# Kernel tuning notes

Measured on AMD Instinct MI355X. Metric: run time of the kernel, lower is better.

Reference implementation:

```python
import jax, jax.numpy as jnp
import numpy as np
from jax import lax


def _dct_basis():
    # 64 separable 2D DCT-II basis filters, shape [64,1,8,8] (OIHW)
    k = 8
    a = np.full(k, np.sqrt(2.0 / k)); a[0] = np.sqrt(1.0 / k)
    u = np.arange(k)[:, None]; xx = np.arange(k)[None, :]
    B = a[:, None] * np.cos((2 * xx + 1) * u * np.pi / (2 * k))  # [u, x]
    basis = np.einsum('ux,vy->uvxy', B, B).reshape(64, 1, k, k)
    return jnp.asarray(basis, dtype=jnp.float32)


def _conv(x, w, b, pad):
    y = lax.conv_general_dilated(x, w, (1, 1), [(pad, pad), (pad, pad)],
                                 dimension_numbers=('NCHW', 'OIHW', 'NCHW'))
    return y + b[None, :, None, None]


def _bn(x, s, b, m, v, eps=1e-5):
    inv = s * lax.rsqrt(v + eps)
    return x * inv[None, :, None, None] + (b - m * inv)[None, :, None, None]


def _mp2(x):
    return lax.reduce_window(x, -jnp.inf, lax.max, (1, 1, 2, 2), (1, 1, 2, 2), 'VALID')


def setup_inputs() -> dict:
    key = jax.random.key(0)
    ks = jax.random.split(key, 32)
    B = 128
    d = {}
    d['x'] = jax.random.normal(ks[0], (B, 1, 256, 256), jnp.float32)
    d['qvectors'] = jax.random.uniform(ks[1], (B, 64), jnp.float32)
    d['dct_basis'] = _dct_basis()
    def w(k, shape, sc=0.02):
        return jax.random.normal(k, shape, jnp.float32) * sc
    # conv stack
    d['conv1a_w'] = w(ks[2], (64, 1, 5, 5));   d['conv1a_b'] = w(ks[3], (64,))
    d['conv1b_w'] = w(ks[4], (64, 64, 5, 5));  d['conv1b_b'] = w(ks[5], (64,))
    d['conv2a_w'] = w(ks[6], (128, 64, 5, 5)); d['conv2a_b'] = w(ks[7], (128,))
    d['conv3a_w'] = w(ks[8], (256, 128, 5, 5)); d['conv3a_b'] = w(ks[9], (256,))
    # batchnorm (eval-mode) params: scale, bias, running_mean, running_var
    for i, (name, c) in enumerate([('bn1a', 64), ('bn1b', 64), ('bn2a', 128), ('bn3a', 256)]):
        kk = jax.random.split(ks[10 + i], 4)
        d[name + '_s'] = 1.0 + w(kk[0], (c,))
        d[name + '_b'] = w(kk[1], (c,))
        d[name + '_m'] = w(kk[2], (c,))
        d[name + '_v'] = jax.random.uniform(kk[3], (c,), jnp.float32, 0.5, 1.5)
    d['fc1_w'] = w(ks[20], (500, 15 * 8 * 256 + 64), 0.01); d['fc1_b'] = w(ks[21], (500,))
    d['fc2_w'] = w(ks[22], (500, 564), 0.01);               d['fc2_b'] = w(ks[23], (500,))
    d['fc3_w'] = w(ks[24], (2, 564), 0.01);                 d['fc3_b'] = w(ks[25], (2,))
    return d


def reference(x, qvectors, dct_basis,
              conv1a_w, conv1a_b, bn1a_s, bn1a_b, bn1a_m, bn1a_v,
              conv1b_w, conv1b_b, bn1b_s, bn1b_b, bn1b_m, bn1b_v,
              conv2a_w, conv2a_b, bn2a_s, bn2a_b, bn2a_m, bn2a_v,
              conv3a_w, conv3a_b, bn3a_s, bn3a_b, bn3a_m, bn3a_v,
              fc1_w, fc1_b, fc2_w, fc2_b, fc3_w, fc3_b):
    gamma = 1e6
    # --- soft-histogram over DCT coefficients (no_grad in the original) ---
    dct = lax.conv_general_dilated(x, dct_basis, (8, 8), 'VALID',
                                   dimension_numbers=('NCHW', 'OIHW', 'NCHW'))  # [B,64,32,32]
    bins = jnp.arange(-60, 61, dtype=jnp.float32)  # 121 bins

    def step(_, b):
        s = jnp.sum(jax.nn.sigmoid(gamma * (dct - b)), axis=(2, 3)) / 1024.0  # [B,64]
        return None, s
    _, feats = lax.scan(step, None, bins)           # [121,B,64]
    feats = jnp.transpose(feats, (1, 0, 2))          # [B,121,64]
    features = feats[:, 0:120, :] - feats[:, 1:121, :]
    features = lax.stop_gradient(features.reshape(-1, 1, 120, 64))

    # --- CNN backbone ---
    h = jax.nn.relu(_bn(_conv(features, conv1a_w, conv1a_b, 2), bn1a_s, bn1a_b, bn1a_m, bn1a_v))
    h = jax.nn.relu(_bn(_conv(h, conv1b_w, conv1b_b, 2), bn1b_s, bn1b_b, bn1b_m, bn1b_v))
    h = _mp2(h)
    h = jax.nn.relu(_bn(_conv(h, conv2a_w, conv2a_b, 2), bn2a_s, bn2a_b, bn2a_m, bn2a_v))
    h = _mp2(h)
    h = jax.nn.relu(_bn(_conv(h, conv3a_w, conv3a_b, 2), bn3a_s, bn3a_b, bn3a_m, bn3a_v))
    h = _mp2(h)                                      # [B,256,15,8]
    h_flat = h.reshape(-1, 15 * 8 * 256)
    h = jnp.concatenate([qvectors, h_flat], axis=1)
    h = jax.nn.relu(h @ fc1_w.T + fc1_b)
    h = jnp.concatenate([qvectors, h], axis=1)
    h = jax.nn.relu(h @ fc2_w.T + fc2_b)
    h = jnp.concatenate([qvectors, h], axis=1)
    return h @ fc3_w.T + fc3_b
```

## Files before the change

kernel.cpp:

```cpp
#include <hip/hip_runtime.h>


typedef _Float16 half8 __attribute__((ext_vector_type(8)));
typedef _Float16 half4 __attribute__((ext_vector_type(4)));
typedef float f32x16 __attribute__((ext_vector_type(16)));

__device__ __forceinline__ void async_copy16(const void* g, void* l) {
  __builtin_amdgcn_global_load_lds(
      (__attribute__((address_space(1))) void*)g,
      (__attribute__((address_space(3))) void*)l, 16, 0, 0);
}

__global__ __launch_bounds__(256) void dct_kernel(const float* __restrict__ x,
                                                  const float* __restrict__ basis,
                                                  float* __restrict__ dct) {
  __shared__ __align__(16) float Bm[64];
  int tid = threadIdx.x;
  if (tid < 64) {
    int u = tid >> 3, xx = tid & 7;
    Bm[tid] = basis[(u * 8) * 64 + xx * 8] * 2.8284271247461903f;
  }
  __syncthreads();
  int gid = blockIdx.x * 256 + tid;
  int b = gid >> 10, blk = gid & 1023;
  int bi = blk >> 5, bj = blk & 31;
  const float* xp = x + (size_t)b * 65536 + (bi * 8) * 256 + bj * 8;
  float X[64];
#pragma unroll
  for (int r = 0; r < 8; ++r) {
    float4 p = *(const float4*)(xp + r * 256);
    float4 q = *(const float4*)(xp + r * 256 + 4);
    X[r * 8 + 0] = p.x; X[r * 8 + 1] = p.y; X[r * 8 + 2] = p.z; X[r * 8 + 3] = p.w;
    X[r * 8 + 4] = q.x; X[r * 8 + 5] = q.y; X[r * 8 + 6] = q.z; X[r * 8 + 7] = q.w;
  }
  float T[64];
#pragma unroll
  for (int u = 0; u < 8; ++u) {
    float t[8] = {0.f, 0.f, 0.f, 0.f, 0.f, 0.f, 0.f, 0.f};
#pragma unroll
    for (int xx = 0; xx < 8; ++xx) {
      float bm = Bm[u * 8 + xx];
#pragma unroll
      for (int y = 0; y < 8; ++y) t[y] += bm * X[xx * 8 + y];
    }
#pragma unroll
    for (int y = 0; y < 8; ++y) T[u * 8 + y] = t[y];
  }
  float* op = dct + (size_t)b * 65536 + bi * 32 + bj;
#pragma unroll
  for (int v = 0; v < 8; ++v) {
    float dc[8] = {0.f, 0.f, 0.f, 0.f, 0.f, 0.f, 0.f, 0.f};
#pragma unroll
    for (int y = 0; y < 8; ++y) {
      float bm = Bm[v * 8 + y];
#pragma unroll
      for (int u = 0; u < 8; ++u) dc[u] += bm * T[u * 8 + y];
    }
#pragma unroll
    for (int u = 0; u < 8; ++u) op[(u * 8 + v) * 1024] = dc[u];
  }
}

__global__ __launch_bounds__(256) void hist_kernel(const float* __restrict__ dct,
                                                   float* __restrict__ feat) {
  __shared__ __align__(16) float h[16 * 121];
  int tid = threadIdx.x;
  for (int i = tid; i < 16 * 121; i += 256) h[i] = 0.f;
  __syncthreads();
  int b = blockIdx.x >> 6, c = blockIdx.x & 63;
  const float* dp = dct + (size_t)(b * 64 + c) * 1024;
  float* hc = h + (tid & 15) * 121;
  float4 v4 = ((const float4*)dp)[tid];
  float vals[4] = {v4.x, v4.y, v4.z, v4.w};
#pragma unroll
  for (int i = 0; i < 4; ++i) {
    float d = vals[i];
    float fl = floorf(d);
    float t0 = d - fl;
    int k = (int)fl + 60;
    if (t0 >= 2e-5f && t0 <= 1.f - 1.2e-4f) {
      if (k >= 0 && k < 120) atomicAdd(hc + k, 1.0f);
    } else {
      float s0 = 1.f / (1.f + expf(-1e6f * t0));
      float s1 = 1.f / (1.f + expf(1e6f * (1.f - t0)));
      if (k >= 1 && k <= 120) atomicAdd(hc + k - 1, 1.f - s0);
      if (k >= 0 && k < 120)  atomicAdd(hc + k, s0 - s1);
      if (k >= -1 && k < 119) atomicAdd(hc + k + 1, s1);
    }
  }
  __syncthreads();
  for (int f = tid; f < 120; f += 256) {
    float s = 0.f;
#pragma unroll
    for (int l = 0; l < 16; ++l) s += h[l * 121 + f];
    feat[((size_t)b * 120 + f) * 64 + c] = s * (1.f / 1024.f);
  }
}

template <int CI, int CO>
__global__ __launch_bounds__(256) void wtrans(const float* __restrict__ w,
                                              _Float16* __restrict__ wt) {
  int i = blockIdx.x * 256 + threadIdx.x;
  if (i >= (CI / 8) * 26 * CO * 8) return;
  int c8 = i & 7;
  int t = i >> 3;
  int co = t % CO; t /= CO;
  int k = t % 26;
  int cg = t / 26;
  int ci = cg * 8 + c8;
  float v = (k < 25) ? w[((size_t)co * CI + ci) * 25 + k] : 0.f;
  wt[i] = (_Float16)v;
}

__global__ __launch_bounds__(256) void bnprep(const float* __restrict__ cb,
                                              const float* __restrict__ s,
                                              const float* __restrict__ b,
                                              const float* __restrict__ m,
                                              const float* __restrict__ v,
                                              float* __restrict__ scale,
                                              float* __restrict__ shift, int n) {
  int i = threadIdx.x;
  if (i < n) {
    float inv = s[i] * rsqrtf(v[i] + 1e-5f);
    scale[i] = inv;
    shift[i] = (cb[i] - m[i]) * inv + b[i];
  }
}

__global__ __launch_bounds__(256) void conv1a_f16(
    const float* __restrict__ in, const float* __restrict__ wts,
    const float* __restrict__ cb, const float* __restrict__ s_,
    const float* __restrict__ b_, const float* __restrict__ m_,
    const float* __restrict__ v_, _Float16* __restrict__ out) {
  __shared__ __align__(16) float wl[5 * 8 * 20];
  __shared__ __align__(16) float il[12 * 68];
  int tid = threadIdx.x, bid = blockIdx.x;
  int img = bid / 30;
  int r = bid % 30;
  int cob = r / 15;
  int h0 = (r % 15) * 8;
  int cog = tid & 7, wg = (tid >> 3) & 3, hh = tid >> 5;
  float acc[4][16];
#pragma unroll
  for (int i = 0; i < 4; ++i)
#pragma unroll
    for (int j = 0; j < 16; ++j) acc[i][j] = 0.f;
  for (int idx = tid; idx < 32 * 25; idx += 256) {
    int rr = idx % 25, co = idx / 25;
    float v = wts[(cob * 32 + co) * 25 + rr];
    int kh = rr / 5, kw = rr % 5;
    wl[(kh * 8 + (co >> 2)) * 20 + (co & 3) * 5 + kw] = v;
  }
  for (int idx = tid; idx < 12 * 68; idx += 256) {
    int cc = idx % 68, rr = idx / 68;
    int hy = h0 + rr - 2, wx = cc - 2;
    float v = 0.f;
    if (hy >= 0 && hy < 120 && wx >= 0 && wx < 64)
      v = in[(size_t)img * 7680 + hy * 64 + wx];
    il[idx] = v;
  }
  __syncthreads();
#pragma unroll
  for (int kh = 0; kh < 5; ++kh) {
    const float* ir = &il[(hh + kh) * 68 + wg * 16];
    float iv[20];
#pragma unroll
    for (int i = 0; i < 5; ++i) {
      float4 p = *(const float4*)(ir + i * 4);
      iv[i * 4] = p.x; iv[i * 4 + 1] = p.y; iv[i * 4 + 2] = p.z; iv[i * 4 + 3] = p.w;
    }
    const float* wr = &wl[(kh * 8 + cog) * 20];
    float wv[20];
#pragma unroll
    for (int i = 0; i < 5; ++i) {
      float4 p = *(const float4*)(wr + i * 4);
      wv[i * 4] = p.x; wv[i * 4 + 1] = p.y; wv[i * 4 + 2] = p.z; wv[i * 4 + 3] = p.w;
    }
#pragma unroll
    for (int co = 0; co < 4; ++co)
#pragma unroll
      for (int kw = 0; kw < 5; ++kw) {
        float w1 = wv[co * 5 + kw];
#pragma unroll
        for (int w = 0; w < 16; ++w) acc[co][w] += w1 * iv[w + kw];
      }
  }
  int h = h0 + hh;
  int co0 = cob * 32 + cog * 4;
  float inv[4], bia[4];
#pragma unroll
  for (int i = 0; i < 4; ++i) {
    int c = co0 + i;
    inv[i] = s_[c] * rsqrtf(v_[c] + 1e-5f);
    bia[i] = (cb[c] - m_[c]) * inv[i] + b_[c];
  }
  int g = co0 >> 3, off = co0 & 7;
  _Float16* op = out + (((size_t)(img * 8 + g) * 120 + h) * 64) * 8 + off;
#pragma unroll
  for (int w = 0; w < 16; ++w) {
    half4 o;
#pragma unroll
    for (int i = 0; i < 4; ++i)
      o[i] = (_Float16)fmaxf(acc[i][w] * inv[i] + bia[i], 0.f);
    *(half4*)&op[(size_t)(wg * 16 + w) * 8] = o;
  }
}

template <int CI, int CO, int H, int W, int BLK_M, bool OUT_NCHW, bool DBUF>
__global__ __launch_bounds__(512) void conv5_mfma(
    const _Float16* __restrict__ in, const _Float16* __restrict__ wt,
    const float* __restrict__ scale, const float* __restrict__ shift,
    _Float16* __restrict__ out) {
  constexpr int NW_M = BLK_M / 64;
  constexpr int NW_N = 8 / NW_M;
  constexpr int BLK_N = NW_N * 128;
  constexpr int ROWS = BLK_N / W;
  constexpr int TB = (H + ROWS - 1) / ROWS;
  constexpr int NCOB = CO / BLK_M;
  constexpr int HR = ROWS + 4;
  constexpr int HC = W + 4;
  constexpr int CIG = CI / 8;
  constexpr int OH = H / 2, OW = W / 2;
  constexpr int AITER = (HR * HC + 511) / 512;
  constexpr int WBYTES = 26 * BLK_M * 16;
  constexpr int WITER = (WBYTES + 8191) / 8192;
  constexpr int NBUF = DBUF ? 2 : 1;
  constexpr int ASZ = HR * HC * 8;
  constexpr int WSZ = 26 * BLK_M * 8;
  __shared__ __align__(16) _Float16 Alds[NBUF][ASZ];
  __shared__ __align__(16) _Float16 Wlds[NBUF][WSZ];

  int tid = threadIdx.x;
  int bid = blockIdx.x;
  int img = bid / (TB * NCOB);
  int r = bid % (TB * NCOB);
  int tb = r / NCOB;
  int cob = r % NCOB;
  int h0 = tb * ROWS;

  int wid = tid >> 6, l = tid & 63, lo = l & 31, hi = l >> 5;
  int widM = wid / NW_N, widN = wid % NW_N;

  int wbase[2];
#pragma unroll
  for (int mi = 0; mi < 2; ++mi)
    wbase[mi] = (hi * BLK_M + widM * 64 + mi * 32 + lo) * 8;
  int bbase[4];
#pragma unroll
  for (int j = 0; j < 4; ++j) {
    int pix = widN * 128 + j * 32 + lo;
    bbase[j] = ((pix / W) * HC + (pix % W)) * 8;
  }

  f32x16 acc[2][4];
#pragma unroll
  for (int mi = 0; mi < 2; ++mi)
#pragma unroll
    for (int j = 0; j < 4; ++j) acc[mi][j] = (f32x16){};

  auto loadA = [&](int cg, half8* areg) {
    const _Float16* ing = in + (size_t)(img * CIG + cg) * H * W * 8;
#pragma unroll
    for (int it = 0; it < AITER; ++it) {
      int i = tid + it * 512;
      half8 v = {};
      if (i < HR * HC) {
        int rr = i / HC, cc = i % HC;
        int hy = h0 + rr - 2, wx = cc - 2;
        if (hy >= 0 && hy < H && wx >= 0 && wx < W)
          v = *(const half8*)&ing[(size_t)(hy * W + wx) * 8];
      }
      areg[it] = v;
    }
  };
  auto issueW = [&](int cg, int buf) {
    const char* wsrc = (const char*)(wt + ((size_t)cg * 26 * CO + cob * BLK_M) * 8);
#pragma unroll
    for (int rr = 0; rr < WITER; ++rr) {
      int f = rr * 8192 + tid * 16;
      if (f < WBYTES) {
        int row = f / (BLK_M * 16);
        int off = f % (BLK_M * 16);
        async_copy16(wsrc + (size_t)row * (CO * 16) + off,
                     (char*)&Wlds[buf][0] + (rr * 8192 + wid * 1024));
      }
    }
  };
  auto writeA = [&](int buf, half8* areg) {
#pragma unroll
    for (int it = 0; it < AITER; ++it) {
      int i = tid + it * 512;
      if (i < HR * HC) *(half8*)&Alds[buf][i * 8] = areg[it];
    }
  };
  auto ldfrag = [&](int buf, int p, half8 (&af)[2], half8 (&bf)[4]) {
    int pos0 = 2 * p, pos1 = 2 * p + 1;
    int off0 = (pos0 / 5) * HC + (pos0 % 5);
    int off1 = (pos1 < 25) ? (pos1 / 5) * HC + (pos1 % 5) : 0;
    int off = (hi ? off1 : off0) * 8;
#pragma unroll
    for (int mi = 0; mi < 2; ++mi)
      af[mi] = *(const half8*)&Wlds[buf][wbase[mi] + pos0 * BLK_M * 8];
#pragma unroll
    for (int j = 0; j < 4; ++j)
      bf[j] = *(const half8*)&Alds[buf][bbase[j] + off];
  };
  auto compute = [&](int buf) {
    half8 afA[2], bfA[4], afB[2], bfB[4];
    ldfrag(buf, 0, afA, bfA);
#pragma unroll
    for (int p = 0; p < 13; ++p) {
      const bool even = (p & 1) == 0;
      if (p + 1 < 13) {
        if (even) ldfrag(buf, p + 1, afB, bfB);
        else      ldfrag(buf, p + 1, afA, bfA);
      }
      __builtin_amdgcn_s_setprio(1);
#pragma unroll
      for (int mi = 0; mi < 2; ++mi)
#pragma unroll
        for (int j = 0; j < 4; ++j)
          acc[mi][j] = __builtin_amdgcn_mfma_f32_32x32x16_f16(
              even ? afA[mi] : afB[mi], even ? bfA[j] : bfB[j],
              acc[mi][j], 0, 0, 0);
      __builtin_amdgcn_s_setprio(0);
    }
  };

  if constexpr (DBUF) {
    half8 areg[AITER];
    loadA(0, areg);
    issueW(0, 0);
    writeA(0, areg);
    __syncthreads();
#pragma unroll 1
    for (int cg = 0; cg < CIG; ++cg) {
      int cur = cg & 1;
      if (cg + 1 < CIG) {
        loadA(cg + 1, areg);
        issueW(cg + 1, cur ^ 1);
      }
      compute(cur);
      if (cg + 1 < CIG) writeA(cur ^ 1, areg);
      __syncthreads();
    }
  } else {
#pragma unroll 1
    for (int cg = 0; cg < CIG; ++cg) {
      half8 areg[AITER];
      loadA(cg, areg);
      issueW(cg, 0);
      writeA(0, areg);
      __syncthreads();
      compute(0);
      __syncthreads();
    }
  }

  if (!OUT_NCHW) {
    constexpr int CGO = CO / 8;
    int gbase = (cob * BLK_M + widM * 64) >> 3;
    bool lane_ok = ((lo & 1) == 0);
#pragma unroll
    for (int mi = 0; mi < 2; ++mi) {
#pragma unroll
      for (int r4 = 0; r4 < 4; ++r4) {
        int g = gbase + mi * 4 + r4;
        int co0 = g * 8 + hi * 4;
        float4 sv = *(const float4*)&scale[co0];
        float4 tv = *(const float4*)&shift[co0];
        float sa[4] = {sv.x, sv.y, sv.z, sv.w};
        float ta[4] = {tv.x, tv.y, tv.z, tv.w};
#pragma unroll
        for (int p = 0; p < 2; ++p) {
          int ja = (W == 64) ? p : 2 * p;
          int jb = (W == 64) ? p + 2 : 2 * p + 1;
          int orow = (W == 64) ? (h0 >> 1) + widN : (h0 >> 1) + widN * 2 + p;
          int ocol = (W == 64) ? p * 16 + (lo >> 1) : (lo >> 1);
          half4 o;
#pragma unroll
          for (int c = 0; c < 4; ++c) {
            int reg = r4 * 4 + c;
            float v0 = fmaxf(acc[mi][ja][reg] * sa[c] + ta[c], 0.f);
            float v1 = fmaxf(acc[mi][jb][reg] * sa[c] + ta[c], 0.f);
            float m = fmaxf(v0, v1);
            m = fmaxf(m, __shfl_xor(m, 1, 64));
            o[c] = (_Float16)m;
          }
          if (lane_ok && orow < OH)
            *(half4*)&out[(((size_t)(img * CGO + g) * OH + orow) * OW + ocol) * 8 +
                          hi * 4] = o;
        }
      }
    }
  } else {
    bool lane_ok = ((lo & 1) == 0) && (lo < 16);
#pragma unroll
    for (int mi = 0; mi < 2; ++mi) {
#pragma unroll
      for (int reg = 0; reg < 16; ++reg) {
        int co = cob * BLK_M + widM * 64 + mi * 32 + (reg & 3) + 8 * (reg >> 2) + 4 * hi;
        float s = scale[co], t = shift[co];
#pragma unroll
        for (int j = 0; j < 4; ++j) {
          float v = fmaxf(acc[mi][j][reg] * s + t, 0.f);
          float m = fmaxf(v, __shfl_xor(v, 16, 64));
          m = fmaxf(m, __shfl_xor(m, 1, 64));
          int orow = (h0 >> 1) + widN * 4 + j;
          if (lane_ok && orow < OH)
            out[((size_t)(img * CO + co) * OH + orow) * OW + ((lo & 15) >> 1)] =
                (_Float16)m;
        }
      }
    }
  }
}

__global__ __launch_bounds__(256, 2) void fc1_mfma(const float* __restrict__ qv,
                                                   const _Float16* __restrict__ p3,
                                                   const float* __restrict__ w,
                                                   float* __restrict__ part) {
  __shared__ __align__(16) _Float16 Wl[8 * 256 * 8];
  __shared__ __align__(16) _Float16 Bl[8 * 128 * 8];
  int tid = threadIdx.x;
  int ks = blockIdx.x >> 1, mt = blockIdx.x & 1;
  int wid = tid >> 6, l = tid & 63, lo = l & 31, hi = l >> 5;
  f32x16 acc[2][4];
#pragma unroll
  for (int mi = 0; mi < 2; ++mi)
#pragma unroll
    for (int j = 0; j < 4; ++j) acc[mi][j] = (f32x16){};

#pragma unroll 1
  for (int i3 = 0; i3 < 3; ++i3) {
    int c = ks + 240 * i3;
    if (c > 480) break;
    for (int idx = tid; idx < 2048; idx += 256) {
      int n_loc = idx >> 3, k8 = idx & 7;
      int n = mt * 256 + n_loc;
      half8 v = {};
      if (n < 500) {
        const float* src = w + (size_t)n * 30784 + c * 64 + k8 * 8;
        float4 f0 = *(const float4*)src;
        float4 f1 = *(const float4*)(src + 4);
        v[0] = (_Float16)f0.x; v[1] = (_Float16)f0.y;
        v[2] = (_Float16)f0.z; v[3] = (_Float16)f0.w;
        v[4] = (_Float16)f1.x; v[5] = (_Float16)f1.y;
        v[6] = (_Float16)f1.z; v[7] = (_Float16)f1.w;
      }
      *(half8*)&Wl[(size_t)(k8 * 256 + n_loc) * 8] = v;
    }
    for (int idx = tid; idx < 1024; idx += 256) {
      int img = idx >> 3, k8 = idx & 7;
      half8 v;
      if (c == 0) {
        const float* src = qv + img * 64 + k8 * 8;
        float4 f0 = *(const float4*)src;
        float4 f1 = *(const float4*)(src + 4);
        v[0] = (_Float16)f0.x; v[1] = (_Float16)f0.y;
        v[2] = (_Float16)f0.z; v[3] = (_Float16)f0.w;
        v[4] = (_Float16)f1.x; v[5] = (_Float16)f1.y;
        v[6] = (_Float16)f1.z; v[7] = (_Float16)f1.w;
      } else {
        v = *(const half8*)&p3[(size_t)img * 30720 + (c * 64 - 64) + k8 * 8];
      }
      *(half8*)&Bl[(size_t)(k8 * 128 + img) * 8] = v;
    }
    __syncthreads();
#pragma unroll
    for (int ks16 = 0; ks16 < 4; ++ks16) {
      half8 af[2], bf[4];
#pragma unroll
      for (int mi = 0; mi < 2; ++mi)
        af[mi] = *(const half8*)&Wl[(size_t)((ks16 * 2 + hi) * 256 + wid * 64 +
                                             mi * 32 + lo) * 8];
#pragma unroll
      for (int j = 0; j < 4; ++j)
        bf[j] = *(const half8*)&Bl[(size_t)((ks16 * 2 + hi) * 128 + j * 32 + lo) * 8];
#pragma unroll
      for (int mi = 0; mi < 2; ++mi)
#pragma unroll
        for (int j = 0; j < 4; ++j)
          acc[mi][j] = __builtin_amdgcn_mfma_f32_32x32x16_f16(
              af[mi], bf[j], acc[mi][j], 0, 0, 0);
    }
    __syncthreads();
  }
#pragma unroll
  for (int mi = 0; mi < 2; ++mi)
#pragma unroll
    for (int reg = 0; reg < 16; ++reg) {
      int n = mt * 256 + wid * 64 + mi * 32 + (reg & 3) + 8 * (reg >> 2) + 4 * hi;
#pragma unroll
      for (int j = 0; j < 4; ++j)
        part[((size_t)ks * 512 + n) * 128 + j * 32 + lo] = acc[mi][j][reg];
    }
}

__global__ __launch_bounds__(256) void fc1_reduce(const float* __restrict__ part,
                                                  const float* __restrict__ bias,
                                                  float* __restrict__ out) {
  int idx = blockIdx.x * 256 + threadIdx.x;
  int img = idx & 127, n = idx >> 7;
  float s = 0.f;
#pragma unroll 8
  for (int ks = 0; ks < 240; ++ks) s += part[((size_t)ks * 512 + n) * 128 + img];
  out[n * 128 + img] = (n < 500) ? fmaxf(s + bias[n], 0.f) : 0.f;
}

__global__ __launch_bounds__(256) void fc2_kernel(const float* __restrict__ qv,
                                                  const float* __restrict__ fc1o,
                                                  const float* __restrict__ w,
                                                  const float* __restrict__ bias,
                                                  float* __restrict__ out) {
  int idx = blockIdx.x * 256 + threadIdx.x;
  if (idx >= 128 * 500) return;
  int m = idx & 127, n = idx >> 7;
  const float* wr = w + (size_t)n * 564;
  float acc = 0.f;
#pragma unroll 8
  for (int k = 0; k < 64; ++k) acc += qv[m * 64 + k] * wr[k];
#pragma unroll 4
  for (int k = 0; k < 500; ++k) acc += fc1o[k * 128 + m] * wr[64 + k];
  out[n * 128 + m] = fmaxf(acc + bias[n], 0.f);
}

__global__ __launch_bounds__(256) void fc3_kernel(const float* __restrict__ qv,
                                                  const float* __restrict__ fc2o,
                                                  const float* __restrict__ w,
                                                  const float* __restrict__ bias,
                                                  float* __restrict__ out) {
  int tid = threadIdx.x;
  int m = tid >> 1, n = tid & 1;
  const float* wr = w + (size_t)n * 564;
  float acc = 0.f;
#pragma unroll 8
  for (int k = 0; k < 64; ++k) acc += qv[m * 64 + k] * wr[k];
#pragma unroll 4
  for (int k = 0; k < 500; ++k) acc += fc2o[k * 128 + m] * wr[64 + k];
  out[m * 2 + n] = acc + bias[n];
}

extern "C" void kernel_launch(void* const* d_in, const int* in_sizes, int n_in,
                              void* d_out, int out_size, void* d_ws, size_t ws_size,
                              hipStream_t stream) {
  (void)in_sizes; (void)n_in; (void)out_size; (void)ws_size;
  const float* x      = (const float*)d_in[0];
  const float* qv     = (const float*)d_in[1];
  const float* basis  = (const float*)d_in[2];
  const float* c1aw   = (const float*)d_in[3];
  const float* c1ab   = (const float*)d_in[4];
  const float* c1bw   = (const float*)d_in[5];
  const float* c1bb   = (const float*)d_in[6];
  const float* c2aw   = (const float*)d_in[7];
  const float* c2ab   = (const float*)d_in[8];
  const float* c3aw   = (const float*)d_in[9];
  const float* c3ab   = (const float*)d_in[10];
  const float* bn1a_s = (const float*)d_in[11];
  const float* bn1a_b = (const float*)d_in[12];
  const float* bn1a_m = (const float*)d_in[13];
  const float* bn1a_v = (const float*)d_in[14];
  const float* bn1b_s = (const float*)d_in[15];
  const float* bn1b_b = (const float*)d_in[16];
  const float* bn1b_m = (const float*)d_in[17];
  const float* bn1b_v = (const float*)d_in[18];
  const float* bn2a_s = (const float*)d_in[19];
  const float* bn2a_b = (const float*)d_in[20];
  const float* bn2a_m = (const float*)d_in[21];
  const float* bn2a_v = (const float*)d_in[22];
  const float* bn3a_s = (const float*)d_in[23];
  const float* bn3a_b = (const float*)d_in[24];
  const float* bn3a_m = (const float*)d_in[25];
  const float* bn3a_v = (const float*)d_in[26];
  const float* fc1w   = (const float*)d_in[27];
  const float* fc1b   = (const float*)d_in[28];
  const float* fc2w   = (const float*)d_in[29];
  const float* fc2b   = (const float*)d_in[30];
  const float* fc3w   = (const float*)d_in[31];
  const float* fc3b   = (const float*)d_in[32];

  float* ws = (float*)d_ws;
  float* feat = ws;
  _Float16* wt1b = (_Float16*)(ws + 1000000);
  _Float16* wt2a = (_Float16*)(ws + 1070000);
  _Float16* wt3a = (_Float16*)(ws + 1200000);
  float* sc1b = ws + 1700000; float* sh1b = ws + 1700100;
  float* sc2a = ws + 1700200; float* sh2a = ws + 1700400;
  float* sc3a = ws + 1700600; float* sh3a = ws + 1701000;
  _Float16* p1 = (_Float16*)(ws + 1710000);
  float* S = ws + 9600000;
  float* dct     = S;
  _Float16* a1c  = (_Float16*)S;
  _Float16* p2   = (_Float16*)(ws + 25400000);
  _Float16* p3   = (_Float16*)(ws + 1710000);
  float* f1p  = S;
  float* f1o  = ws + 29400000;
  float* f2o  = ws + 29500000;

  wtrans<64, 64><<<416, 256, 0, stream>>>(c1bw, wt1b);
  wtrans<64, 128><<<832, 256, 0, stream>>>(c2aw, wt2a);
  wtrans<128, 256><<<3328, 256, 0, stream>>>(c3aw, wt3a);
  bnprep<<<1, 256, 0, stream>>>(c1bb, bn1b_s, bn1b_b, bn1b_m, bn1b_v, sc1b, sh1b, 64);
  bnprep<<<1, 256, 0, stream>>>(c2ab, bn2a_s, bn2a_b, bn2a_m, bn2a_v, sc2a, sh2a, 128);
  bnprep<<<1, 256, 0, stream>>>(c3ab, bn3a_s, bn3a_b, bn3a_m, bn3a_v, sc3a, sh3a, 256);

  dct_kernel<<<512, 256, 0, stream>>>(x, basis, dct);
  hist_kernel<<<128 * 64, 256, 0, stream>>>(dct, feat);

  for (int c = 0; c < 2; ++c) {
    const float* fin = feat + (size_t)c * 64 * 120 * 64;
    _Float16* pout = p1 + (size_t)c * 64 * 8 * 60 * 32 * 8;
    conv1a_f16<<<64 * 30, 256, 0, stream>>>(fin, c1aw, c1ab, bn1a_s, bn1a_b,
                                            bn1a_m, bn1a_v, a1c);
    conv5_mfma<64, 64, 120, 64, 64, false, false><<<64 * 8, 512, 0, stream>>>(
        a1c, wt1b, sc1b, sh1b, pout);
  }

  conv5_mfma<64, 128, 60, 32, 128, false, false><<<128 * 4, 512, 0, stream>>>(
      p1, wt2a, sc2a, sh2a, p2);

  conv5_mfma<128, 256, 30, 16, 128, true, false><<<128 * 2, 512, 0, stream>>>(
      p2, wt3a, sc3a, sh3a, p3);

  fc1_mfma<<<480, 256, 0, stream>>>(qv, p3, fc1w, f1p);
  fc1_reduce<<<256, 256, 0, stream>>>(f1p, fc1b, f1o);
  fc2_kernel<<<250, 256, 0, stream>>>(qv, f1o, fc2w, fc2b, f2o);
  fc3_kernel<<<1, 256, 0, stream>>>(qv, f2o, fc3w, fc3b, (float*)d_out);
}
```

Before: 779.2 us.

## Fuse DCT with histogram binning and halve fc1 split-K partitions

The DCT kernel now bins its coefficients directly into per-block shared-memory histograms, two copies per block, and writes partial histograms that a small reduce kernel sums into features. This removes the 32 MB DCT intermediate round-trip and the separate histogram kernel. The cost is about 61 KB of LDS per block, which can limit occupancy, plus more shared-memory atomic contention. Separately, fc1 now uses 120 K-splits instead of 240, so each block does more work and the partial-sum buffer and reduce traffic shrink.

```diff
diff --git a/kernel.cpp b/kernel.cpp
--- a/kernel.cpp
+++ b/kernel.cpp
@@ -11,18 +11,21 @@
       (__attribute__((address_space(3))) void*)l, 16, 0, 0);
 }
 
-__global__ __launch_bounds__(256) void dct_kernel(const float* __restrict__ x,
-                                                  const float* __restrict__ basis,
-                                                  float* __restrict__ dct) {
+__global__ __launch_bounds__(256) void dcthist_kernel(const float* __restrict__ x,
+                                                      const float* __restrict__ basis,
+                                                      float* __restrict__ hpart) {
   __shared__ __align__(16) float Bm[64];
+  __shared__ float Hl[2 * 64 * 120];
   int tid = threadIdx.x;
   if (tid < 64) {
     int u = tid >> 3, xx = tid & 7;
     Bm[tid] = basis[(u * 8) * 64 + xx * 8] * 2.8284271247461903f;
   }
+  for (int i = tid; i < 2 * 64 * 120; i += 256) Hl[i] = 0.f;
   __syncthreads();
-  int gid = blockIdx.x * 256 + tid;
-  int b = gid >> 10, blk = gid & 1023;
+  int gb = blockIdx.x;
+  int b = gb >> 2;
+  int blk = (gb & 3) * 256 + tid;
   int bi = blk >> 5, bj = blk & 31;
   const float* xp = x + (size_t)b * 65536 + (bi * 8) * 256 + bj * 8;
   float X[64];
@@ -46,9 +49,11 @@
 #pragma unroll
     for (int y = 0; y < 8; ++y) T[u * 8 + y] = t[y];
   }
-  float* op = dct + (size_t)b * 65536 + bi * 32 + bj;
-#pragma unroll
-  for (int v = 0; v < 8; ++v) {
+  int vr = tid & 7;
+  float* Hs = Hl + ((tid >> 3) & 1) * (64 * 120);
+#pragma unroll 1
+  for (int vv = 0; vv < 8; ++vv) {
+    int v = (vv + vr) & 7;
     float dc[8] = {0.f, 0.f, 0.f, 0.f, 0.f, 0.f, 0.f, 0.f};
 #pragma unroll
     for (int y = 0; y < 8; ++y) {
@@ -57,44 +62,38 @@
       for (int u = 0; u < 8; ++u) dc[u] += bm * T[u * 8 + y];
     }
 #pragma unroll
-    for (int u = 0; u < 8; ++u) op[(u * 8 + v) * 1024] = dc[u];
-  }
-}
-
-__global__ __launch_bounds__(256) void hist_kernel(const float* __restrict__ dct,
+    for (int u = 0; u < 8; ++u) {
+      float d = dc[u];
+      float* hc = Hs + (u * 8 + v) * 120;
+      float fl = floorf(d);
+      float t0 = d - fl;
+      int k = (int)fl + 60;
+      if (t0 >= 2e-5f && t0 <= 1.f - 1.2e-4f) {
+        if (k >= 0 && k < 120) atomicAdd(hc + k, 1.0f);
+      } else {
+        float s0 = 1.f / (1.f + expf(-1e6f * t0));
+        float s1 = 1.f / (1.f + expf(1e6f * (1.f - t0)));
+        if (k >= 1 && k <= 120) atomicAdd(hc + k - 1, 1.f - s0);
+        if (k >= 0 && k < 120)  atomicAdd(hc + k, s0 - s1);
+        if (k >= -1 && k < 119) atomicAdd(hc + k + 1, s1);
+      }
+    }
+  }
+  __syncthreads();
+  for (int i = tid; i < 7680; i += 256) {
+    int f = i >> 6, c = i & 63;
+    hpart[(size_t)gb * 7680 + i] = Hl[c * 120 + f] + Hl[64 * 120 + c * 120 + f];
+  }
+}
+
+__global__ __launch_bounds__(256) void hist_reduce(const float* __restrict__ hpart,
                                                    float* __restrict__ feat) {
-  __shared__ __align__(16) float h[16 * 121];
-  int tid = threadIdx.x;
-  for (int i = tid; i < 16 * 121; i += 256) h[i] = 0.f;
-  __syncthreads();
-  int b = blockIdx.x >> 6, c = blockIdx.x & 63;
-  const float* dp = dct + (size_t)(b * 64 + c) * 1024;
-  float* hc = h + (tid & 15) * 121;
-  float4 v4 = ((const float4*)dp)[tid];
-  float vals[4] = {v4.x, v4.y, v4.z, v4.w};
-#pragma unroll
-  for (int i = 0; i < 4; ++i) {
-    float d = vals[i];
-    float fl = floorf(d);
-    float t0 = d - fl;
-    int k = (int)fl + 60;
-    if (t0 >= 2e-5f && t0 <= 1.f - 1.2e-4f) {
-      if (k >= 0 && k < 120) atomicAdd(hc + k, 1.0f);
-    } else {
-      float s0 = 1.f / (1.f + expf(-1e6f * t0));
-      float s1 = 1.f / (1.f + expf(1e6f * (1.f - t0)));
-      if (k >= 1 && k <= 120) atomicAdd(hc + k - 1, 1.f - s0);
-      if (k >= 0 && k < 120)  atomicAdd(hc + k, s0 - s1);
-      if (k >= -1 && k < 119) atomicAdd(hc + k + 1, s1);
-    }
-  }
-  __syncthreads();
-  for (int f = tid; f < 120; f += 256) {
-    float s = 0.f;
-#pragma unroll
-    for (int l = 0; l < 16; ++l) s += h[l * 121 + f];
-    feat[((size_t)b * 120 + f) * 64 + c] = s * (1.f / 1024.f);
-  }
+  int idx = blockIdx.x * 256 + threadIdx.x;
+  int b = idx / 7680, r = idx - b * 7680;
+  float s = 0.f;
+#pragma unroll
+  for (int q = 0; q < 4; ++q) s += hpart[(size_t)(b * 4 + q) * 7680 + r];
+  feat[(size_t)b * 7680 + r] = s * (1.f / 1024.f);
 }
 
 template <int CI, int CO>
@@ -432,8 +431,8 @@
     for (int j = 0; j < 4; ++j) acc[mi][j] = (f32x16){};
 
 #pragma unroll 1
-  for (int i3 = 0; i3 < 3; ++i3) {
-    int c = ks + 240 * i3;
+  for (int i3 = 0; i3 < 5; ++i3) {
+    int c = ks + 120 * i3;
     if (c > 480) break;
     for (int idx = tid; idx < 2048; idx += 256) {
       int n_loc = idx >> 3, k8 = idx & 7;
@@ -504,7 +503,7 @@
   int img = idx & 127, n = idx >> 7;
   float s = 0.f;
 #pragma unroll 8
-  for (int ks = 0; ks < 240; ++ks) s += part[((size_t)ks * 512 + n) * 128 + img];
+  for (int ks = 0; ks < 120; ++ks) s += part[((size_t)ks * 512 + n) * 128 + img];
   out[n * 128 + img] = (n < 500) ? fmaxf(s + bias[n], 0.f) : 0.f;
 }
 
@@ -589,7 +588,7 @@
   float* sc3a = ws + 1700600; float* sh3a = ws + 1701000;
   _Float16* p1 = (_Float16*)(ws + 1710000);
   float* S = ws + 9600000;
-  float* dct     = S;
+  float* hpart   = S;
   _Float16* a1c  = (_Float16*)S;
   _Float16* p2   = (_Float16*)(ws + 25400000);
   _Float16* p3   = (_Float16*)(ws + 1710000);
@@ -604,8 +603,8 @@
   bnprep<<<1, 256, 0, stream>>>(c2ab, bn2a_s, bn2a_b, bn2a_m, bn2a_v, sc2a, sh2a, 128);
   bnprep<<<1, 256, 0, stream>>>(c3ab, bn3a_s, bn3a_b, bn3a_m, bn3a_v, sc3a, sh3a, 256);
 
-  dct_kernel<<<512, 256, 0, stream>>>(x, basis, dct);
-  hist_kernel<<<128 * 64, 256, 0, stream>>>(dct, feat);
+  dcthist_kernel<<<512, 256, 0, stream>>>(x, basis, hpart);
+  hist_reduce<<<3840, 256, 0, stream>>>(hpart, feat);
 
   for (int c = 0; c < 2; ++c) {
     const float* fin = feat + (size_t)c * 64 * 120 * 64;
@@ -622,7 +621,7 @@
   conv5_mfma<128, 256, 30, 16, 128, true, false><<<128 * 2, 512, 0, stream>>>(
       p2, wt3a, sc3a, sh3a, p3);
 
-  fc1_mfma<<<480, 256, 0, stream>>>(qv, p3, fc1w, f1p);
+  fc1_mfma<<<240, 256, 0, stream>>>(qv, p3, fc1w, f1p);
   fc1_reduce<<<256, 256, 0, stream>>>(f1p, fc1b, f1o);
   fc2_kernel<<<250, 256, 0, stream>>>(qv, f1o, fc2w, fc2b, f2o);
   fc3_kernel<<<1, 256, 0, stream>>>(qv, f2o, fc3w, fc3b, (float*)d_out);
```

Result: no change. 768.6 us (-1.4%).
